# Optimization experiments

Hardware: AMD Instinct MI355X
Metric: run time of the kernel (lower is better)

The kernel has to match this reference:

```python
import jax, jax.numpy as jnp
import numpy as np

EMBED = 512
HID = 512
MAXMEM = 65536
THRESH = 0.5
EPS = 1e-12  # F.normalize eps


def setup_inputs() -> dict:
    key = jax.random.key(0)
    ks = jax.random.split(key, 10)
    s = 1.0 / np.sqrt(HID)
    return {
        "keys": jax.random.normal(ks[0], (2, 1024, EMBED), jnp.float32),
        "values": jax.random.normal(ks[1], (2, 1024, EMBED), jnp.float32),
        "attention_scores": jax.random.uniform(ks[2], (2, 1024), jnp.float32),
        "query_embeddings": jax.random.normal(ks[3], (256, EMBED), jnp.float32),
        "keys_mem": jnp.zeros((MAXMEM, EMBED), jnp.float32),
        "values_mem": jnp.zeros((MAXMEM, EMBED), jnp.float32),
        "W_ih": jax.random.uniform(ks[4], (4 * HID, EMBED), jnp.float32, -s, s),
        "W_hh": jax.random.uniform(ks[5], (4 * HID, HID), jnp.float32, -s, s),
        "b_ih": jax.random.uniform(ks[6], (4 * HID,), jnp.float32, -s, s),
        "b_hh": jax.random.uniform(ks[7], (4 * HID,), jnp.float32, -s, s),
        "W_out": jax.random.uniform(ks[8], (EMBED, HID), jnp.float32, -s, s),
        "b_out": jnp.zeros((EMBED,), jnp.float32),
        "top_k": 8,
    }


def _lstm(xs, W_ih, W_hh, b_ih, b_hh):
    # single-layer LSTM over sequence xs: (N, E) -> (N, H), torch gate order i,f,g,o
    H = W_hh.shape[1]
    b = b_ih + b_hh
    def step(carry, x):
        h, c = carry
        g = x @ W_ih.T + h @ W_hh.T + b  # (4H,)
        i, f, gg, o = jnp.split(g, 4)
        c = jax.nn.sigmoid(f) * c + jax.nn.sigmoid(i) * jnp.tanh(gg)
        h = jax.nn.sigmoid(o) * jnp.tanh(c)
        return (h, c), h
    h0 = jnp.zeros((H,), xs.dtype)
    (_, _), hs = jax.lax.scan(step, (h0, h0), xs)
    return hs


def reference(keys, values, attention_scores, query_embeddings, keys_mem, values_mem,
              W_ih, W_hh, b_ih, b_hh, W_out, b_out, top_k):
    E = keys.shape[-1]
    M = keys_mem.shape[0]
    k_flat = keys.reshape(-1, E)
    v_flat = values.reshape(-1, E)
    s_flat = attention_scores.reshape(-1)
    N = k_flat.shape[0]

    # --- update_memory: compact selected tokens to the front (stable), run LSTM,
    # then circular-buffer scatter of the first n_sel outputs (write_index starts at 0).
    mask = s_flat > THRESH
    order = jnp.argsort(jnp.logical_not(mask), stable=True)  # selected first, order preserved
    n_sel = jnp.sum(mask)
    ks = k_flat[order]
    vs = v_flat[order]
    hs = _lstm(ks, W_ih, W_hh, b_ih, b_hh)       # (N, H); first n_sel rows match LSTM on compacted seq
    mem_out = hs @ W_out.T + b_out               # (N, E)

    pos = jnp.arange(N)
    idx = jnp.where(pos < n_sel, pos % M, M)     # M = out-of-range sentinel -> dropped
    keys_mem = keys_mem.at[idx].set(mem_out, mode='drop')
    values_mem = values_mem.at[idx].set(vs, mode='drop')
    current_size = jnp.minimum(n_sel, M)

    # --- retrieve_memory: cosine-similarity top-k over the valid prefix of the bank.
    qn = query_embeddings / jnp.maximum(
        jnp.linalg.norm(query_embeddings, axis=1, keepdims=True), EPS)
    kn = keys_mem / jnp.maximum(jnp.linalg.norm(keys_mem, axis=1, keepdims=True), EPS)
    sims = qn @ kn.T                              # (B, M)
    valid = jnp.arange(M)[None, :] < current_size
    sims = jnp.where(valid, sims, -jnp.inf)
    _, topk_idx = jax.lax.top_k(sims, top_k)      # (B, top_k)
    retrieved = values_mem[topk_idx]              # (B, top_k, E)
    return retrieved
```

## Files before the change

kernel.cpp:

```cpp
#include <hip/hip_runtime.h>
#include <math.h>

#define SENT 2.0f
#define NTOK 2048
#define EDIM 512
#define GJ   2048
#define NW   32
#define HPW  16
#define LOG2E 1.4426950408889634f

typedef float f32x4 __attribute__((ext_vector_type(4)));

__device__ __forceinline__ float sigm_f(float x) {
  return __builtin_amdgcn_rcpf(1.f + __builtin_amdgcn_exp2f(-LOG2E * x));
}
__device__ __forceinline__ float tanh_f(float x) {
  return 1.f - 2.f * __builtin_amdgcn_rcpf(1.f + __builtin_amdgcn_exp2f(2.f * LOG2E * x));
}

__global__ __launch_bounds__(256) void k_init(float4* __restrict__ H4) {
  int i = blockIdx.x * blockDim.x + threadIdx.x;
  H4[i] = make_float4(SENT, SENT, SENT, SENT);
}

__global__ __launch_bounds__(1024) void k_compact(const float* __restrict__ scores,
                                                  int* __restrict__ sel,
                                                  int* __restrict__ nselp) {
  __shared__ int cnt[1024];
  const int tid = threadIdx.x;
  const int i0 = tid * 2, i1 = tid * 2 + 1;
  const int m0 = (scores[i0] > 0.5f) ? 1 : 0;
  const int m1 = (scores[i1] > 0.5f) ? 1 : 0;
  cnt[tid] = m0 + m1;
  __syncthreads();
  for (int off = 1; off < 1024; off <<= 1) {
    int v = cnt[tid];
    int u = (tid >= off) ? cnt[tid - off] : 0;
    __syncthreads();
    cnt[tid] = v + u;
    __syncthreads();
  }
  int excl = (tid == 0) ? 0 : cnt[tid - 1];
  if (m0) sel[excl] = i0;
  if (m1) sel[excl + m0] = i1;
  if (tid == 1023) *nselp = cnt[1023];
}

template<bool GATHER>
__global__ __launch_bounds__(256) void k_gemm(
    const float* __restrict__ A, const float* __restrict__ B,
    const float* __restrict__ bias1, const float* __restrict__ bias2,
    float* __restrict__ C, const int* __restrict__ sel,
    const int* __restrict__ nselp, int J)
{
  const int n_sel = *nselp;
  const int t0 = blockIdx.x * 32;
  if (t0 >= n_sel) return;
  const int j0 = blockIdx.y * 64;
  const int tid = threadIdx.x;
  __shared__ float As[32][36];
  __shared__ float Bst[32][68];
  __shared__ int rowsrc[32];
  if (tid < 32) {
    int t = t0 + tid;
    int r = -1;
    if (t < n_sel) r = GATHER ? sel[t] : t;
    rowsrc[tid] = r;
  }
  __syncthreads();
  const int tx = tid & 15;
  const int ty = tid >> 4;
  float4 acc0 = make_float4(0.f, 0.f, 0.f, 0.f);
  float4 acc1 = make_float4(0.f, 0.f, 0.f, 0.f);
  for (int e0 = 0; e0 < EDIM; e0 += 32) {
    {
      int t = tid >> 3, e4 = tid & 7;
      int r = rowsrc[t];
      float4 v = make_float4(0.f, 0.f, 0.f, 0.f);
      if (r >= 0) v = ((const float4*)(A + (size_t)r * EDIM + e0))[e4];
      *(float4*)&As[t][e4 * 4] = v;
    }
    #pragma unroll
    for (int l = 0; l < 2; ++l) {
      int idx = tid + l * 256;
      int j = idx >> 3, e4 = idx & 7;
      float4 v = ((const float4*)(B + (size_t)(j0 + j) * EDIM + e0))[e4];
      Bst[e4 * 4 + 0][j] = v.x; Bst[e4 * 4 + 1][j] = v.y;
      Bst[e4 * 4 + 2][j] = v.z; Bst[e4 * 4 + 3][j] = v.w;
    }
    __syncthreads();
    #pragma unroll
    for (int e = 0; e < 32; ++e) {
      float a0 = As[ty * 2 + 0][e];
      float a1 = As[ty * 2 + 1][e];
      float4 b = *(const float4*)&Bst[e][tx * 4];
      acc0.x += a0 * b.x; acc0.y += a0 * b.y; acc0.z += a0 * b.z; acc0.w += a0 * b.w;
      acc1.x += a1 * b.x; acc1.y += a1 * b.y; acc1.z += a1 * b.z; acc1.w += a1 * b.w;
    }
    __syncthreads();
  }
  float4 bv = ((const float4*)bias1)[(j0 >> 2) + tx];
  if (bias2) {
    float4 b2 = ((const float4*)bias2)[(j0 >> 2) + tx];
    bv.x += b2.x; bv.y += b2.y; bv.z += b2.z; bv.w += b2.w;
  }
  #pragma unroll
  for (int i = 0; i < 2; ++i) {
    int t = t0 + ty * 2 + i;
    if (t < n_sel) {
      float4 a = (i == 0) ? acc0 : acc1;
      float4 r = make_float4(a.x + bv.x, a.y + bv.y, a.z + bv.z, a.w + bv.w);
      *(float4*)(C + (size_t)t * J + j0 + tx * 4) = r;
    }
  }
}

__global__ __launch_bounds__(512, 1) void k_lstm(
    const float* __restrict__ Gin, float* __restrict__ Hout,
    const float* __restrict__ Whh, const int* __restrict__ nselp)
{
  const int tid = threadIdx.x;
  const int n_sel = *nselp;
  if (n_sel <= 0) return;
  const int w = blockIdx.x;

  const int row_local = tid >> 3;
  const int sub = tid & 7;
  const int g = row_local >> 4;
  const int jl = row_local & 15;
  const int grow = g * 512 + w * HPW + jl;
  const int c0 = sub * 64;
  float4 wv[16];
  {
    const float4* wp = (const float4*)(Whh + (size_t)grow * 512 + c0);
    #pragma unroll
    for (int k = 0; k < 16; ++k) wv[k] = wp[(k + sub) & 15];
  }

  const int q = (tid < 128) ? tid : -1;
  const bool ownq = (q >= w * 4 && q < w * 4 + 4);
  const bool gatel = (tid >= 128 && tid < 128 + HPW);
  const int u = tid - 128;

  __shared__ float hl[512];
  __shared__ float gsum[64];
  float cst = 0.f;
  float gx0 = 0.f, gx1 = 0.f, gx2 = 0.f, gx3 = 0.f;
  if (gatel) {
    const float* gr = Gin + w * HPW + u;
    gx0 = gr[0]; gx1 = gr[512]; gx2 = gr[1024]; gx3 = gr[1536];
    hl[w * HPW + u] = 0.f;
  }
  for (int t = 0; t < n_sel; ++t) {
    float nx0 = 0.f, nx1 = 0.f, nx2 = 0.f, nx3 = 0.f;
    if (gatel && t + 1 < n_sel) {
      const float* gr = Gin + (size_t)(t + 1) * GJ + w * HPW + u;
      nx0 = gr[0]; nx1 = gr[512]; nx2 = gr[1024]; nx3 = gr[1536];
    }
    if (q >= 0 && !ownq) {
      if (t == 0) {
        *(float4*)&hl[q * 4] = make_float4(0.f, 0.f, 0.f, 0.f);
      } else {
        const float* src = Hout + (size_t)(t - 1) * 512 + q * 4;
        float a, b, c2, d;
        do {
          a  = __hip_atomic_load(src + 0, __ATOMIC_RELAXED, __HIP_MEMORY_SCOPE_AGENT);
          b  = __hip_atomic_load(src + 1, __ATOMIC_RELAXED, __HIP_MEMORY_SCOPE_AGENT);
          c2 = __hip_atomic_load(src + 2, __ATOMIC_RELAXED, __HIP_MEMORY_SCOPE_AGENT);
          d  = __hip_atomic_load(src + 3, __ATOMIC_RELAXED, __HIP_MEMORY_SCOPE_AGENT);
        } while (a == SENT || b == SENT || c2 == SENT || d == SENT);
        hl[q * 4 + 0] = a; hl[q * 4 + 1] = b;
        hl[q * 4 + 2] = c2; hl[q * 4 + 3] = d;
      }
    }
    __syncthreads();
    const float4* hv = (const float4*)&hl[c0];
    float s0 = 0.f, s1 = 0.f, s2 = 0.f, s3 = 0.f;
    #pragma unroll
    for (int k = 0; k < 4; ++k) {
      float4 w4, h4;
      w4 = wv[4*k+0]; h4 = hv[(4*k+0+sub)&15]; s0 += w4.x*h4.x + w4.y*h4.y + w4.z*h4.z + w4.w*h4.w;
      w4 = wv[4*k+1]; h4 = hv[(4*k+1+sub)&15]; s1 += w4.x*h4.x + w4.y*h4.y + w4.z*h4.z + w4.w*h4.w;
      w4 = wv[4*k+2]; h4 = hv[(4*k+2+sub)&15]; s2 += w4.x*h4.x + w4.y*h4.y + w4.z*h4.z + w4.w*h4.w;
      w4 = wv[4*k+3]; h4 = hv[(4*k+3+sub)&15]; s3 += w4.x*h4.x + w4.y*h4.y + w4.z*h4.z + w4.w*h4.w;
    }
    float s = (s0 + s1) + (s2 + s3);
    s += __shfl_xor(s, 1); s += __shfl_xor(s, 2); s += __shfl_xor(s, 4);
    if (sub == 0) gsum[row_local] = s;
    __syncthreads();
    if (gatel) {
      float gi = gx0 + gsum[u];
      float gf = gx1 + gsum[16 + u];
      float gg = gx2 + gsum[32 + u];
      float go = gx3 + gsum[48 + u];
      float ig = sigm_f(gi);
      float fg = sigm_f(gf);
      float og = sigm_f(go);
      cst = fg * cst + ig * tanh_f(gg);
      float h = og * tanh_f(cst);
      __hip_atomic_store(Hout + (size_t)t * 512 + w * HPW + u, h,
                         __ATOMIC_RELAXED, __HIP_MEMORY_SCOPE_AGENT);
      hl[w * HPW + u] = h;
      gx0 = nx0; gx1 = nx1; gx2 = nx2; gx3 = nx3;
    }
  }
}

__global__ __launch_bounds__(256) void k_norms(
    const float* __restrict__ memo, const float* __restrict__ qe,
    float* __restrict__ dens, const int* __restrict__ nselp)
{
  const int n_sel = *nselp;
  const int row = blockIdx.x * 4 + (threadIdx.x >> 6);
  const int lane = threadIdx.x & 63;
  const float* src;
  if (row < NTOK) {
    if (row >= n_sel) return;
    src = memo + (size_t)row * EDIM;
  } else {
    if (row >= NTOK + 256) return;
    src = qe + (size_t)(row - NTOK) * EDIM;
  }
  const float4* s4 = (const float4*)src;
  float4 a = s4[lane], b = s4[lane + 64];
  float s = a.x*a.x + a.y*a.y + a.z*a.z + a.w*a.w
          + b.x*b.x + b.y*b.y + b.z*b.z + b.w*b.w;
  #pragma unroll
  for (int off = 32; off; off >>= 1) s += __shfl_xor(s, off);
  if (lane == 0) dens[row] = fmaxf(sqrtf(s), 1e-12f);
}

__global__ __launch_bounds__(256) void k_retrieve(
    const float* __restrict__ memo, const float* __restrict__ qe,
    const float* __restrict__ dens, const float* __restrict__ values,
    const int* __restrict__ sel, const int* __restrict__ nselp,
    float* __restrict__ out, int top_k)
{
  const int n_sel = *nselp;
  const int qb = blockIdx.x * 4;
  const int tid = threadIdx.x;
  __shared__ float qs[4][EDIM];
  __shared__ float sims[4][NTOK];
  __shared__ int tix[4][8];
  for (int l = tid; l < 512; l += 256) {
    int q = l >> 7, e4 = l & 127;
    float4 v = ((const float4*)(qe + (size_t)(qb + q) * EDIM))[e4];
    float inv = 1.f / dens[NTOK + qb + q];
    v.x *= inv; v.y *= inv; v.z *= inv; v.w *= inv;
    *(float4*)&qs[q][e4 * 4] = v;
  }
  __syncthreads();
  for (int t = tid; t < n_sel; t += 256) {
    const float4* m4 = (const float4*)(memo + (size_t)t * EDIM);
    float a0 = 0.f, a1 = 0.f, a2 = 0.f, a3 = 0.f;
    for (int e4 = 0; e4 < 128; ++e4) {
      float4 m = m4[e4];
      float4 q0 = *(const float4*)&qs[0][e4 * 4];
      float4 q1 = *(const float4*)&qs[1][e4 * 4];
      float4 q2 = *(const float4*)&qs[2][e4 * 4];
      float4 q3 = *(const float4*)&qs[3][e4 * 4];
      a0 += m.x*q0.x + m.y*q0.y + m.z*q0.z + m.w*q0.w;
      a1 += m.x*q1.x + m.y*q1.y + m.z*q1.z + m.w*q1.w;
      a2 += m.x*q2.x + m.y*q2.y + m.z*q2.z + m.w*q2.w;
      a3 += m.x*q3.x + m.y*q3.y + m.z*q3.z + m.w*q3.w;
    }
    float inv = 1.f / dens[t];
    sims[0][t] = a0 * inv; sims[1][t] = a1 * inv;
    sims[2][t] = a2 * inv; sims[3][t] = a3 * inv;
  }
  __syncthreads();
  const int wq = tid >> 6, lane = tid & 63;
  for (int r = 0; r < top_k; ++r) {
    if (r < n_sel) {
      float bv = -INFINITY; int bi = 0x7fffffff;
      for (int t = lane; t < n_sel; t += 64) {
        float v = sims[wq][t];
        if (v > bv || (v == bv && t < bi)) { bv = v; bi = t; }
      }
      #pragma unroll
      for (int off = 32; off; off >>= 1) {
        float ov = __shfl_xor(bv, off);
        int   oi = __shfl_xor(bi, off);
        if (ov > bv || (ov == bv && oi < bi)) { bv = ov; bi = oi; }
      }
      if (lane == 0) { tix[wq][r] = bi; sims[wq][bi] = -INFINITY; }
    } else if (lane == 0) {
      tix[wq][r] = -1;
    }
    __syncthreads();
  }
  const int tot = 4 * top_k * 128;
  for (int l = tid; l < tot; l += 256) {
    int q = l / (top_k * 128);
    int rem = l - q * top_k * 128;
    int r = rem >> 7;
    int e4 = rem & 127;
    int t = tix[q][r];
    float4 v = make_float4(0.f, 0.f, 0.f, 0.f);
    if (t >= 0) v = ((const float4*)(values + (size_t)sel[t] * EDIM))[e4];
    ((float4*)out)[(((size_t)(qb + q) * top_k) + r) * 128 + e4] = v;
  }
}

extern "C" void kernel_launch(void* const* d_in, const int* in_sizes, int n_in,
                              void* d_out, int out_size, void* d_ws, size_t ws_size,
                              hipStream_t stream) {
  const float* keys   = (const float*)d_in[0];
  const float* values = (const float*)d_in[1];
  const float* scores = (const float*)d_in[2];
  const float* qe     = (const float*)d_in[3];
  const float* W_ih   = (const float*)d_in[6];
  const float* W_hh   = (const float*)d_in[7];
  const float* b_ih   = (const float*)d_in[8];
  const float* b_hh   = (const float*)d_in[9];
  const float* W_out  = (const float*)d_in[10];
  const float* b_out  = (const float*)d_in[11];
  float* out = (float*)d_out;
  const int top_k = out_size / (256 * 512);

  char* ws = (char*)d_ws;
  int*   nsel   = (int*)ws;
  int*   sel    = (int*)(ws + 4096);
  float* dens   = (float*)(ws + 16384);
  float* Hout   = (float*)(ws + (size_t)(1u << 20));
  float* Gin    = (float*)(ws + (size_t)(9u << 20));
  float* memo   = (float*)(ws + (size_t)(9u << 20));
  (void)in_sizes; (void)n_in; (void)ws_size;

  k_init<<<1024, 256, 0, stream>>>((float4*)Hout);
  k_compact<<<1, 1024, 0, stream>>>(scores, sel, nsel);
  k_gemm<true ><<<dim3(64, 32), 256, 0, stream>>>(keys, W_ih, b_ih, b_hh, Gin, sel, nsel, GJ);
  k_lstm<<<NW, 512, 0, stream>>>(Gin, Hout, W_hh, nsel);
  k_gemm<false><<<dim3(64, 8), 256, 0, stream>>>(Hout, W_out, b_out, nullptr, memo, nullptr, nsel, EDIM);
  k_norms<<<576, 256, 0, stream>>>(memo, qe, dens, nsel);
  k_retrieve<<<64, 256, 0, stream>>>(memo, qe, dens, values, sel, nsel, out, top_k);
}
```

Measured before the change: 1.914 ms.

## Remove second barrier in LSTM step via in-wave gate reduction and double-buffered h

Remaps W_hh rows so the four gates of each hidden unit sit in the same wavefront, letting the gate sums be gathered with shuffles instead of a shared-memory array and a second __syncthreads per timestep. The hidden-state buffer is double-buffered to avoid write-after-read hazards once that barrier is gone. Cross-block polling of the previous h is rewritten in inline assembly that keeps two sets of cache-bypassing loads in flight, to cut spin latency. This adds hand-written ISA and ties correctness to the exact row/lane mapping and the sentinel value.

```diff
diff --git a/kernel.cpp b/kernel.cpp
--- a/kernel.cpp
+++ b/kernel.cpp
@@ -126,8 +126,8 @@
 
   const int row_local = tid >> 3;
   const int sub = tid & 7;
-  const int g = row_local >> 4;
-  const int jl = row_local & 15;
+  const int g = row_local & 3;
+  const int jl = row_local >> 2;
   const int grow = g * 512 + w * HPW + jl;
   const int c0 = sub * 64;
   float4 wv[16];
@@ -137,44 +137,77 @@
     for (int k = 0; k < 16; ++k) wv[k] = wp[(k + sub) & 15];
   }
 
-  const int q = (tid < 128) ? tid : -1;
-  const bool ownq = (q >= w * 4 && q < w * 4 + 4);
-  const bool gatel = (tid >= 128 && tid < 128 + HPW);
-  const int u = tid - 128;
-
-  __shared__ float hl[512];
-  __shared__ float gsum[64];
+  const bool gatel = (tid & 31) == 0;
+  const int u = tid >> 5;
+  const bool pol = (tid & 1) && (tid < 256);
+  const int q = pol ? ((tid - 1) >> 1) : -1;
+  const bool pact = pol && (q < 4 * w || q >= 4 * w + 4);
+
+  __shared__ float hbuf[2][512];
+  hbuf[0][tid] = 0.f;
   float cst = 0.f;
   float gx0 = 0.f, gx1 = 0.f, gx2 = 0.f, gx3 = 0.f;
   if (gatel) {
     const float* gr = Gin + w * HPW + u;
     gx0 = gr[0]; gx1 = gr[512]; gx2 = gr[1024]; gx3 = gr[1536];
-    hl[w * HPW + u] = 0.f;
   }
   for (int t = 0; t < n_sel; ++t) {
+    const int cur = t & 1;
     float nx0 = 0.f, nx1 = 0.f, nx2 = 0.f, nx3 = 0.f;
     if (gatel && t + 1 < n_sel) {
       const float* gr = Gin + (size_t)(t + 1) * GJ + w * HPW + u;
       nx0 = gr[0]; nx1 = gr[512]; nx2 = gr[1024]; nx3 = gr[1536];
     }
-    if (q >= 0 && !ownq) {
-      if (t == 0) {
-        *(float4*)&hl[q * 4] = make_float4(0.f, 0.f, 0.f, 0.f);
-      } else {
-        const float* src = Hout + (size_t)(t - 1) * 512 + q * 4;
-        float a, b, c2, d;
-        do {
-          a  = __hip_atomic_load(src + 0, __ATOMIC_RELAXED, __HIP_MEMORY_SCOPE_AGENT);
-          b  = __hip_atomic_load(src + 1, __ATOMIC_RELAXED, __HIP_MEMORY_SCOPE_AGENT);
-          c2 = __hip_atomic_load(src + 2, __ATOMIC_RELAXED, __HIP_MEMORY_SCOPE_AGENT);
-          d  = __hip_atomic_load(src + 3, __ATOMIC_RELAXED, __HIP_MEMORY_SCOPE_AGENT);
-        } while (a == SENT || b == SENT || c2 == SENT || d == SENT);
-        hl[q * 4 + 0] = a; hl[q * 4 + 1] = b;
-        hl[q * 4 + 2] = c2; hl[q * 4 + 3] = d;
-      }
-    }
-    __syncthreads();
-    const float4* hv = (const float4*)&hl[c0];
+    if (t > 0 && pact) {
+      const float* src = Hout + (size_t)(t - 1) * 512 + q * 4;
+      float a0, a1, a2, a3, b0, b1, b2, b3, m;
+      asm volatile(
+        "global_load_dword %[a0], %[s], off sc0 sc1\n\t"
+        "global_load_dword %[a1], %[s], off offset:4 sc0 sc1\n\t"
+        "global_load_dword %[a2], %[s], off offset:8 sc0 sc1\n\t"
+        "global_load_dword %[a3], %[s], off offset:12 sc0 sc1\n\t"
+        "global_load_dword %[b0], %[s], off sc0 sc1\n\t"
+        "global_load_dword %[b1], %[s], off offset:4 sc0 sc1\n\t"
+        "global_load_dword %[b2], %[s], off offset:8 sc0 sc1\n\t"
+        "global_load_dword %[b3], %[s], off offset:12 sc0 sc1\n\t"
+        "PL%=:\n\t"
+        "s_waitcnt vmcnt(4)\n\t"
+        "v_max3_f32 %[m], %[a0], %[a1], %[a2]\n\t"
+        "v_max_f32 %[m], %[m], %[a3]\n\t"
+        "v_cmp_lt_f32 vcc, 1.5, %[m]\n\t"
+        "s_cbranch_vccz GA%=\n\t"
+        "global_load_dword %[a0], %[s], off sc0 sc1\n\t"
+        "global_load_dword %[a1], %[s], off offset:4 sc0 sc1\n\t"
+        "global_load_dword %[a2], %[s], off offset:8 sc0 sc1\n\t"
+        "global_load_dword %[a3], %[s], off offset:12 sc0 sc1\n\t"
+        "s_waitcnt vmcnt(4)\n\t"
+        "v_max3_f32 %[m], %[b0], %[b1], %[b2]\n\t"
+        "v_max_f32 %[m], %[m], %[b3]\n\t"
+        "v_cmp_lt_f32 vcc, 1.5, %[m]\n\t"
+        "s_cbranch_vccz GB%=\n\t"
+        "global_load_dword %[b0], %[s], off sc0 sc1\n\t"
+        "global_load_dword %[b1], %[s], off offset:4 sc0 sc1\n\t"
+        "global_load_dword %[b2], %[s], off offset:8 sc0 sc1\n\t"
+        "global_load_dword %[b3], %[s], off offset:12 sc0 sc1\n\t"
+        "s_branch PL%=\n\t"
+        "GB%=:\n\t"
+        "s_waitcnt vmcnt(0)\n\t"
+        "v_mov_b32 %[a0], %[b0]\n\t"
+        "v_mov_b32 %[a1], %[b1]\n\t"
+        "v_mov_b32 %[a2], %[b2]\n\t"
+        "v_mov_b32 %[a3], %[b3]\n\t"
+        "GA%=:\n\t"
+        "s_waitcnt vmcnt(0)\n\t"
+        : [a0]"=&v"(a0), [a1]"=&v"(a1), [a2]"=&v"(a2), [a3]"=&v"(a3),
+          [b0]"=&v"(b0), [b1]"=&v"(b1), [b2]"=&v"(b2), [b3]"=&v"(b3),
+          [m]"=&v"(m)
+        : [s]"v"(src)
+        : "vcc", "memory");
+      hbuf[cur][q * 4 + 0] = a0; hbuf[cur][q * 4 + 1] = a1;
+      hbuf[cur][q * 4 + 2] = a2; hbuf[cur][q * 4 + 3] = a3;
+    }
+    __syncthreads();
+    const float4* hv = (const float4*)&hbuf[cur][c0];
     float s0 = 0.f, s1 = 0.f, s2 = 0.f, s3 = 0.f;
     #pragma unroll
     for (int k = 0; k < 4; ++k) {
@@ -186,13 +219,15 @@
     }
     float s = (s0 + s1) + (s2 + s3);
     s += __shfl_xor(s, 1); s += __shfl_xor(s, 2); s += __shfl_xor(s, 4);
-    if (sub == 0) gsum[row_local] = s;
-    __syncthreads();
+    const int lane = tid & 63;
+    float sf = __shfl(s, lane + 8);
+    float sg = __shfl(s, lane + 16);
+    float so = __shfl(s, lane + 24);
     if (gatel) {
-      float gi = gx0 + gsum[u];
-      float gf = gx1 + gsum[16 + u];
-      float gg = gx2 + gsum[32 + u];
-      float go = gx3 + gsum[48 + u];
+      float gi = gx0 + s;
+      float gf = gx1 + sf;
+      float gg = gx2 + sg;
+      float go = gx3 + so;
       float ig = sigm_f(gi);
       float fg = sigm_f(gf);
       float og = sigm_f(go);
@@ -200,7 +235,7 @@
       float h = og * tanh_f(cst);
       __hip_atomic_store(Hout + (size_t)t * 512 + w * HPW + u, h,
                          __ATOMIC_RELAXED, __HIP_MEMORY_SCOPE_AGENT);
-      hl[w * HPW + u] = h;
+      hbuf[cur ^ 1][w * HPW + u] = h;
       gx0 = nx0; gx1 = nx1; gx2 = nx2; gx3 = nx3;
     }
   }
```

After: 1.826 ms (median of 2 runs). 1.05x faster.
